# Performance work log

Measured on AMD Instinct MI355X. Metric: run time of the kernel, lower is better.

Reference implementation:

```python
import jax, jax.numpy as jnp
import numpy as np

GRID_SIZE = 4
ORDER = 3
NUM_BASIS = GRID_SIZE + ORDER  # 7
KNOTS = jnp.linspace(-1.0, 1.0, NUM_BASIS + ORDER + 1)  # 11 knots


def _normalise(x):
    # eval-mode with uninitialized running stats: use batch min/max
    min_val = x.min(axis=0)
    max_val = x.max(axis=0)
    width = jnp.maximum(max_val - min_val, 0.01)
    centre = 0.5 * (max_val + min_val)
    scaled = (x - centre) / (0.5 * width)
    return jnp.clip(scaled, -2.0, 2.0)


def _bspline_basis(x):
    # x: (B, I) -> basis: (B, I, NUM_BASIS), de Boor recursion vectorized over i
    xe = x[..., None]  # (B, I, 1)
    idx = jnp.arange(NUM_BASIS)
    left, right = KNOTS[idx], KNOTS[idx + 1]
    basis = ((xe >= left) & (xe < right)).astype(x.dtype)
    last = jnp.where(xe[..., 0] == KNOTS[NUM_BASIS], 1.0, basis[..., -1])
    basis = basis.at[..., -1].set(last)
    for k in range(1, ORDER + 1):
        d1 = KNOTS[idx + k] - KNOTS[idx]
        d2 = KNOTS[idx + k + 1] - KNOTS[idx + 1]
        b_next = jnp.concatenate([basis[..., 1:], jnp.zeros_like(basis[..., :1])], axis=-1)
        t1 = jnp.where(d1 > 0, (xe - KNOTS[idx]) / jnp.where(d1 > 0, d1, 1.0), 0.0) * basis
        t2 = jnp.where(d2 > 0, (KNOTS[idx + k + 1] - xe) / jnp.where(d2 > 0, d2, 1.0), 0.0) * b_next
        basis = t1 + t2
    return basis


def setup_inputs() -> dict:
    key = jax.random.key(0)
    k1, k2, k3 = jax.random.split(key, 3)
    B, I, O = 8192, 256, 256
    x = jax.random.normal(k1, (B, I), dtype=jnp.float32)
    # xavier-uniform base_weight
    bound = float(np.sqrt(6.0 / (I + O)))
    base_weight = jax.random.uniform(k2, (O, I), minval=-bound, maxval=bound, dtype=jnp.float32)
    spline_weight = jnp.ones((O, I), dtype=jnp.float32)
    spline_coeff = 0.001 * jax.random.normal(k3, (O, I, NUM_BASIS), dtype=jnp.float32)
    bias = jnp.zeros((O,), dtype=jnp.float32)
    return {"x": x, "base_weight": base_weight, "spline_weight": spline_weight,
            "spline_coeff": spline_coeff, "bias": bias}


def reference(x, base_weight, spline_weight, spline_coeff, bias):
    x_norm = _normalise(x)                          # (B, I)
    basis = _bspline_basis(x_norm)                  # (B, I, M)
    silu_x = x_norm * jax.nn.sigmoid(x_norm)        # (B, I)
    base_out = silu_x @ base_weight.T               # sum_i silu_i * W_oi -> (B, O)
    coeff_scaled = spline_coeff * spline_weight[..., None]  # (O, I, M)
    spline_out = jnp.einsum('bim,oim->bo', basis, coeff_scaled)
    return base_out + spline_out + bias[None, :]
```

## Files before the change

### kernel.cpp

```cpp
#include <hip/hip_runtime.h>
#include <hip/hip_bf16.h>

#define B_SZ 8192
#define I_SZ 256
#define O_SZ 256
#define KDIM 2048
#define BM 32
#define BN 128
#define BKT 64
#define NT 32

typedef __bf16 bf16x8 __attribute__((ext_vector_type(8)));
typedef float f32x4 __attribute__((ext_vector_type(4)));

__global__ __launch_bounds__(256) void minmax_partial(
    const float* __restrict__ x, float* __restrict__ pmin,
    float* __restrict__ pmax) {
  const int cg = threadIdx.x & 63;
  const int rs = threadIdx.x >> 6;
  const int r0 = blockIdx.x * 64;
  const float* p = x + (size_t)(r0 + rs) * I_SZ + cg * 4;
  float4 mn = {1e30f, 1e30f, 1e30f, 1e30f};
  float4 mx = {-1e30f, -1e30f, -1e30f, -1e30f};
#pragma unroll
  for (int k = 0; k < 16; ++k) {
    const float4 v = *reinterpret_cast<const float4*>(p + (size_t)k * 4 * I_SZ);
    mn.x = fminf(mn.x, v.x); mn.y = fminf(mn.y, v.y);
    mn.z = fminf(mn.z, v.z); mn.w = fminf(mn.w, v.w);
    mx.x = fmaxf(mx.x, v.x); mx.y = fmaxf(mx.y, v.y);
    mx.z = fmaxf(mx.z, v.z); mx.w = fmaxf(mx.w, v.w);
  }
  __shared__ float rmn[4][I_SZ], rmx[4][I_SZ];
  *reinterpret_cast<float4*>(&rmn[rs][cg * 4]) = mn;
  *reinterpret_cast<float4*>(&rmx[rs][cg * 4]) = mx;
  __syncthreads();
  if (threadIdx.x < 64) {
    float4 a, b;
    const int c0 = threadIdx.x * 4;
    a.x = fminf(fminf(rmn[0][c0+0], rmn[1][c0+0]), fminf(rmn[2][c0+0], rmn[3][c0+0]));
    a.y = fminf(fminf(rmn[0][c0+1], rmn[1][c0+1]), fminf(rmn[2][c0+1], rmn[3][c0+1]));
    a.z = fminf(fminf(rmn[0][c0+2], rmn[1][c0+2]), fminf(rmn[2][c0+2], rmn[3][c0+2]));
    a.w = fminf(fminf(rmn[0][c0+3], rmn[1][c0+3]), fminf(rmn[2][c0+3], rmn[3][c0+3]));
    b.x = fmaxf(fmaxf(rmx[0][c0+0], rmx[1][c0+0]), fmaxf(rmx[2][c0+0], rmx[3][c0+0]));
    b.y = fmaxf(fmaxf(rmx[0][c0+1], rmx[1][c0+1]), fmaxf(rmx[2][c0+1], rmx[3][c0+1]));
    b.z = fmaxf(fmaxf(rmx[0][c0+2], rmx[1][c0+2]), fmaxf(rmx[2][c0+2], rmx[3][c0+2]));
    b.w = fmaxf(fmaxf(rmx[0][c0+3], rmx[1][c0+3]), fmaxf(rmx[2][c0+3], rmx[3][c0+3]));
    *reinterpret_cast<float4*>(&pmin[blockIdx.x * I_SZ + c0]) = a;
    *reinterpret_cast<float4*>(&pmax[blockIdx.x * I_SZ + c0]) = b;
  }
}

__global__ void pack_W(const float* __restrict__ bw,
                       const float* __restrict__ sw,
                       const float* __restrict__ coeff,
                       __hip_bfloat16* __restrict__ W,
                       const float* __restrict__ pmin,
                       const float* __restrict__ pmax,
                       float* __restrict__ cenrhw) {
  const int idx = blockIdx.x * blockDim.x + threadIdx.x;
  const int i = idx & (I_SZ - 1);
  const int o = idx >> 8;
  const float s = sw[idx];
  union { __hip_bfloat16 h[8]; float4 f4; } u;
#pragma unroll
  for (int m = 0; m < 7; ++m)
    u.h[m] = __float2bfloat16(coeff[(size_t)idx * 7 + m] * s);
  u.h[7] = __float2bfloat16(bw[idx]);
  const size_t off = (size_t)o * KDIM + (size_t)((i ^ (o & 7)) << 3);
  *reinterpret_cast<float4*>(&W[off]) = u.f4;

  if (blockIdx.x == 0) {
    const int c = threadIdx.x;
    float mn = 1e30f, mx = -1e30f;
#pragma unroll 8
    for (int p = 0; p < 128; ++p) {
      mn = fminf(mn, pmin[p * I_SZ + c]);
      mx = fmaxf(mx, pmax[p * I_SZ + c]);
    }
    const float width = fmaxf(mx - mn, 0.01f);
    cenrhw[2 * c]     = 0.5f * (mx + mn);
    cenrhw[2 * c + 1] = 2.0f / width;
  }
}

__device__ __forceinline__ void async16(const __hip_bfloat16* g, __hip_bfloat16* l) {
  __builtin_amdgcn_global_load_lds(
      (const __attribute__((address_space(1))) void*)g,
      (__attribute__((address_space(3))) void*)l, 16, 0, 0);
}

__global__ __launch_bounds__(256, 2) void gemm_fused(
    const float* __restrict__ x, const __hip_bfloat16* __restrict__ W,
    const float* __restrict__ cenrhw, const float* __restrict__ bias,
    float* __restrict__ out) {
  __shared__ __align__(16) __hip_bfloat16 Alds[2][BM * BKT];
  __shared__ __align__(16) __hip_bfloat16 Blds[2][BN * BKT];
  __shared__ float2 scl[I_SZ];

  const int t = threadIdx.x;
  const int lane = t & 63;
  const int wave = t >> 6;
  const int fr = lane & 15, fk = lane >> 4;

  const int bid = blockIdx.x;
  const int swz = (bid & 7) * 64 + (bid >> 3);
  const int bm = swz >> 1, bn = swz & 1;
  const int r0 = bm * BM;
  const int c0 = bn * BN;

  scl[t] = reinterpret_cast<const float2*>(cenrhw)[t];

  const int arow = t >> 3;
  const int af_  = t & 7;
  const float* xp = x + (size_t)(r0 + arow) * I_SZ + af_;

  const __hip_bfloat16* gb0 = W + (size_t)(c0 + (t >> 3)) * KDIM + (t & 7) * 8;

  f32x4 acc[2][2] = {{{0.f,0.f,0.f,0.f},{0.f,0.f,0.f,0.f}},
                     {{0.f,0.f,0.f,0.f},{0.f,0.f,0.f,0.f}}};

  auto stageB = [&](int buf, int kt) {
    const size_t k0 = (size_t)kt * BKT;
    async16(gb0 + k0,                      &Blds[buf][t * 8]);
    async16(gb0 + k0 + (size_t)32 * KDIM,  &Blds[buf][2048 + t * 8]);
    async16(gb0 + k0 + (size_t)64 * KDIM,  &Blds[buf][4096 + t * 8]);
    async16(gb0 + k0 + (size_t)96 * KDIM,  &Blds[buf][6144 + t * 8]);
  };

  auto buildA = [&](int buf, int kt, float xv) {
    const int i = kt * 8 + af_;
    const float2 s = scl[i];
    float xn = (xv - s.x) * s.y;
    xn = fminf(fmaxf(xn, -2.0f), 2.0f);
    float d[11];
#pragma unroll
    for (int j = 0; j < 11; ++j) d[j] = xn - (-1.0f + 0.2f * j);
    float bas[7];
#pragma unroll
    for (int j = 0; j < 7; ++j)
      bas[j] = (d[j] >= 0.0f && d[j + 1] < 0.0f) ? 1.0f : 0.0f;
    if (d[7] == 0.0f) bas[6] = 1.0f;
#pragma unroll
    for (int k = 1; k <= 3; ++k) {
      const float rk = (k == 1) ? 5.0f : (k == 2) ? 2.5f : (1.0f / 0.6f);
#pragma unroll
      for (int j = 0; j < 7; ++j) {
        const float bn_ = (j < 6) ? bas[j + 1] : 0.0f;
        bas[j] = (d[j] * bas[j] - d[j + k + 1] * bn_) * rk;
      }
    }
    const float silu = xn / (1.0f + __expf(-xn));
    union { __hip_bfloat16 h[8]; float4 f4; } u;
#pragma unroll
    for (int m = 0; m < 7; ++m) u.h[m] = __float2bfloat16(bas[m]);
    u.h[7] = __float2bfloat16(silu);
    const int unit = af_ ^ (arow & 7);
    *reinterpret_cast<float4*>(&Alds[buf][arow * BKT + unit * 8]) = u.f4;
  };

  auto compute = [&](int buf) {
    bf16x8 af[2][2], bg[2][2];
#pragma unroll
    for (int m = 0; m < 2; ++m)
#pragma unroll
      for (int kk = 0; kk < 2; ++kk) {
        const int row = m * 16 + fr;
        const int unit = ((kk << 2) | fk) ^ (row & 7);
        af[m][kk] = *reinterpret_cast<const bf16x8*>(&Alds[buf][row * BKT + unit * 8]);
      }
#pragma unroll
    for (int n = 0; n < 2; ++n)
#pragma unroll
      for (int kk = 0; kk < 2; ++kk) {
        const int row = wave * 32 + n * 16 + fr;
        const int unit = ((kk << 2) | fk) ^ (row & 7);
        bg[n][kk] = *reinterpret_cast<const bf16x8*>(&Blds[buf][row * BKT + unit * 8]);
      }
#pragma unroll
    for (int kk = 0; kk < 2; ++kk)
#pragma unroll
      for (int m = 0; m < 2; ++m)
#pragma unroll
        for (int n = 0; n < 2; ++n)
          acc[m][n] = __builtin_amdgcn_mfma_f32_16x16x32_bf16(
              af[m][kk], bg[n][kk], acc[m][n], 0, 0, 0);
  };

  const float xv0 = xp[0];
  float xpf = xp[8];
  __syncthreads();
  stageB(0, 0);
  buildA(0, 0, xv0);
  __syncthreads();
  int cur = 0;
  for (int kt = 0; kt < NT - 1; ++kt) {
    stageB(cur ^ 1, kt + 1);
    float xpf2 = (kt + 2 < NT) ? xp[(kt + 2) * 8] : 0.0f;
    buildA(cur ^ 1, kt + 1, xpf);
    compute(cur);
    __syncthreads();
    xpf = xpf2;
    cur ^= 1;
  }
  compute(cur);

#pragma unroll
  for (int m = 0; m < 2; ++m)
#pragma unroll
    for (int n = 0; n < 2; ++n) {
      const int col = c0 + wave * 32 + n * 16 + fr;
      const float bc = bias[col];
#pragma unroll
      for (int r = 0; r < 4; ++r) {
        const int row = r0 + m * 16 + fk * 4 + r;
        out[(size_t)row * O_SZ + col] = acc[m][n][r] + bc;
      }
    }
}

extern "C" void kernel_launch(void* const* d_in, const int* in_sizes, int n_in,
                              void* d_out, int out_size, void* d_ws, size_t ws_size,
                              hipStream_t stream) {
  const float* x     = (const float*)d_in[0];
  const float* bw    = (const float*)d_in[1];
  const float* sw    = (const float*)d_in[2];
  const float* coeff = (const float*)d_in[3];
  const float* bias  = (const float*)d_in[4];
  float* out = (float*)d_out;

  char* ws = (char*)d_ws;
  __hip_bfloat16* Wbuf = (__hip_bfloat16*)ws;
  float* pmin   = (float*)(ws + (size_t)O_SZ * KDIM * 2);
  float* pmax   = pmin + 128 * I_SZ;
  float* cenrhw = pmax + 128 * I_SZ;

  minmax_partial<<<128, 256, 0, stream>>>(x, pmin, pmax);
  pack_W<<<(O_SZ * I_SZ) / 256, 256, 0, stream>>>(bw, sw, coeff, Wbuf,
                                                  pmin, pmax, cenrhw);
  gemm_fused<<<(B_SZ / BM) * (O_SZ / BN), 256, 0, stream>>>(x, Wbuf, cenrhw,
                                                            bias, out);
}
```

Measured before the change: 47.27 us.

## Use closed-form cubic B-spline, atomic min/max reduction, and lighter barriers

The de Boor recursion in the A-tile builder is replaced by a closed-form uniform cubic B-spline: the normalised value is mapped to a knot interval and the four nonzero basis weights are computed directly. The two-level min/max reduction becomes order-preserving integer atomics, which removes the serial final reduction from pack_W but adds two memsets. The K-loop's __syncthreads is replaced by explicit waitcnt plus s_barrier, which allows one outstanding global load to remain in flight. The aim is to cut ALU work in buildA and shorten the serial reduction step, at the risk of subtle edge-case differences at the clamp boundaries (for example x at exactly the last knot) and of synchronisation correctness.

```diff
diff --git a/kernel.cpp b/kernel.cpp
--- a/kernel.cpp
+++ b/kernel.cpp
@@ -13,9 +13,18 @@
 typedef __bf16 bf16x8 __attribute__((ext_vector_type(8)));
 typedef float f32x4 __attribute__((ext_vector_type(4)));
 
+__device__ __forceinline__ unsigned fkey(float f) {
+  unsigned u = __float_as_uint(f);
+  return (u & 0x80000000u) ? ~u : (u | 0x80000000u);
+}
+__device__ __forceinline__ float funkey(unsigned k) {
+  unsigned u = (k & 0x80000000u) ? (k ^ 0x80000000u) : ~k;
+  return __uint_as_float(u);
+}
+
 __global__ __launch_bounds__(256) void minmax_partial(
-    const float* __restrict__ x, float* __restrict__ pmin,
-    float* __restrict__ pmax) {
+    const float* __restrict__ x, unsigned* __restrict__ smin,
+    unsigned* __restrict__ smax) {
   const int cg = threadIdx.x & 63;
   const int rs = threadIdx.x >> 6;
   const int r0 = blockIdx.x * 64;
@@ -35,28 +44,23 @@
   *reinterpret_cast<float4*>(&rmx[rs][cg * 4]) = mx;
   __syncthreads();
   if (threadIdx.x < 64) {
-    float4 a, b;
-    const int c0 = threadIdx.x * 4;
-    a.x = fminf(fminf(rmn[0][c0+0], rmn[1][c0+0]), fminf(rmn[2][c0+0], rmn[3][c0+0]));
-    a.y = fminf(fminf(rmn[0][c0+1], rmn[1][c0+1]), fminf(rmn[2][c0+1], rmn[3][c0+1]));
-    a.z = fminf(fminf(rmn[0][c0+2], rmn[1][c0+2]), fminf(rmn[2][c0+2], rmn[3][c0+2]));
-    a.w = fminf(fminf(rmn[0][c0+3], rmn[1][c0+3]), fminf(rmn[2][c0+3], rmn[3][c0+3]));
-    b.x = fmaxf(fmaxf(rmx[0][c0+0], rmx[1][c0+0]), fmaxf(rmx[2][c0+0], rmx[3][c0+0]));
-    b.y = fmaxf(fmaxf(rmx[0][c0+1], rmx[1][c0+1]), fmaxf(rmx[2][c0+1], rmx[3][c0+1]));
-    b.z = fmaxf(fmaxf(rmx[0][c0+2], rmx[1][c0+2]), fmaxf(rmx[2][c0+2], rmx[3][c0+2]));
-    b.w = fmaxf(fmaxf(rmx[0][c0+3], rmx[1][c0+3]), fmaxf(rmx[2][c0+3], rmx[3][c0+3]));
-    *reinterpret_cast<float4*>(&pmin[blockIdx.x * I_SZ + c0]) = a;
-    *reinterpret_cast<float4*>(&pmax[blockIdx.x * I_SZ + c0]) = b;
+#pragma unroll
+    for (int c = 0; c < 4; ++c) {
+      const int col = threadIdx.x * 4 + c;
+      const float a = fminf(fminf(rmn[0][col], rmn[1][col]),
+                            fminf(rmn[2][col], rmn[3][col]));
+      const float b = fmaxf(fmaxf(rmx[0][col], rmx[1][col]),
+                            fmaxf(rmx[2][col], rmx[3][col]));
+      atomicMin(&smin[col], fkey(a));
+      atomicMax(&smax[col], fkey(b));
+    }
   }
 }
 
 __global__ void pack_W(const float* __restrict__ bw,
                        const float* __restrict__ sw,
                        const float* __restrict__ coeff,
-                       __hip_bfloat16* __restrict__ W,
-                       const float* __restrict__ pmin,
-                       const float* __restrict__ pmax,
-                       float* __restrict__ cenrhw) {
+                       __hip_bfloat16* __restrict__ W) {
   const int idx = blockIdx.x * blockDim.x + threadIdx.x;
   const int i = idx & (I_SZ - 1);
   const int o = idx >> 8;
@@ -68,19 +72,6 @@
   u.h[7] = __float2bfloat16(bw[idx]);
   const size_t off = (size_t)o * KDIM + (size_t)((i ^ (o & 7)) << 3);
   *reinterpret_cast<float4*>(&W[off]) = u.f4;
-
-  if (blockIdx.x == 0) {
-    const int c = threadIdx.x;
-    float mn = 1e30f, mx = -1e30f;
-#pragma unroll 8
-    for (int p = 0; p < 128; ++p) {
-      mn = fminf(mn, pmin[p * I_SZ + c]);
-      mx = fmaxf(mx, pmax[p * I_SZ + c]);
-    }
-    const float width = fmaxf(mx - mn, 0.01f);
-    cenrhw[2 * c]     = 0.5f * (mx + mn);
-    cenrhw[2 * c + 1] = 2.0f / width;
-  }
 }
 
 __device__ __forceinline__ void async16(const __hip_bfloat16* g, __hip_bfloat16* l) {
@@ -91,8 +82,8 @@
 
 __global__ __launch_bounds__(256, 2) void gemm_fused(
     const float* __restrict__ x, const __hip_bfloat16* __restrict__ W,
-    const float* __restrict__ cenrhw, const float* __restrict__ bias,
-    float* __restrict__ out) {
+    const unsigned* __restrict__ smin, const unsigned* __restrict__ smax,
+    const float* __restrict__ bias, float* __restrict__ out) {
   __shared__ __align__(16) __hip_bfloat16 Alds[2][BM * BKT];
   __shared__ __align__(16) __hip_bfloat16 Blds[2][BN * BKT];
   __shared__ float2 scl[I_SZ];
@@ -108,7 +99,13 @@
   const int r0 = bm * BM;
   const int c0 = bn * BN;
 
-  scl[t] = reinterpret_cast<const float2*>(cenrhw)[t];
+  {
+    const float mn = funkey(smin[t]);
+    const float mx = funkey(smax[t]);
+    const float w = fmaxf(mx - mn, 0.01f);
+    const float rhw = 2.0f / w;
+    scl[t] = make_float2(rhw, -0.5f * (mx + mn) * rhw);
+  }
 
   const int arow = t >> 3;
   const int af_  = t & 7;
@@ -128,37 +125,43 @@
   };
 
   auto buildA = [&](int buf, int kt, float xv) {
-    const int i = kt * 8 + af_;
-    const float2 s = scl[i];
-    float xn = (xv - s.x) * s.y;
-    xn = fminf(fmaxf(xn, -2.0f), 2.0f);
-    float d[11];
-#pragma unroll
-    for (int j = 0; j < 11; ++j) d[j] = xn - (-1.0f + 0.2f * j);
-    float bas[7];
-#pragma unroll
-    for (int j = 0; j < 7; ++j)
-      bas[j] = (d[j] >= 0.0f && d[j + 1] < 0.0f) ? 1.0f : 0.0f;
-    if (d[7] == 0.0f) bas[6] = 1.0f;
-#pragma unroll
-    for (int k = 1; k <= 3; ++k) {
-      const float rk = (k == 1) ? 5.0f : (k == 2) ? 2.5f : (1.0f / 0.6f);
-#pragma unroll
-      for (int j = 0; j < 7; ++j) {
-        const float bn_ = (j < 6) ? bas[j + 1] : 0.0f;
-        bas[j] = (d[j] * bas[j] - d[j + k + 1] * bn_) * rk;
-      }
+    const float2 s2 = scl[kt * 8 + af_];
+    const float xn = __builtin_fmaf(xv, s2.x, s2.y);
+    const float sp = __builtin_fmaf(xn, 5.0f, 5.0f);
+    const float cf = floorf(sp);
+    const float c6 = fminf(cf, 6.0f);
+    const int ci = (int)c6;
+    const float u = sp - c6;
+    const float zm = (sp > 7.0f) ? 0.0f : (1.0f / 6.0f);
+    const float u2 = u * u;
+    const float u3 = u2 * u;
+    const float t1 = 1.0f - u;
+    const float q3 = u3 * zm;
+    const float q0 = (t1 * t1) * (t1 * zm);
+    float h2 = __builtin_fmaf(-3.0f, u, 3.0f);
+    h2 = __builtin_fmaf(h2, u, 3.0f);
+    h2 = __builtin_fmaf(h2, u, 1.0f);
+    const float q2 = h2 * zm;
+    float h1 = __builtin_fmaf(3.0f, u, -6.0f);
+    h1 = __builtin_fmaf(h1, u2, 4.0f);
+    const float q1 = h1 * zm;
+    const float silu = xn * __builtin_amdgcn_rcpf(1.0f + __expf(-xn));
+    union { __hip_bfloat16 h[8]; float4 f4; } uu;
+#pragma unroll
+    for (int j = 0; j < 7; ++j) {
+      float v = 0.0f;
+      v = (ci == j + 3) ? q0 : v;
+      v = (ci == j + 2) ? q1 : v;
+      v = (ci == j + 1) ? q2 : v;
+      v = (ci == j)     ? q3 : v;
+      uu.h[j] = __float2bfloat16(v);
     }
-    const float silu = xn / (1.0f + __expf(-xn));
-    union { __hip_bfloat16 h[8]; float4 f4; } u;
-#pragma unroll
-    for (int m = 0; m < 7; ++m) u.h[m] = __float2bfloat16(bas[m]);
-    u.h[7] = __float2bfloat16(silu);
+    uu.h[7] = __float2bfloat16(silu);
     const int unit = af_ ^ (arow & 7);
-    *reinterpret_cast<float4*>(&Alds[buf][arow * BKT + unit * 8]) = u.f4;
+    *reinterpret_cast<float4*>(&Alds[buf][arow * BKT + unit * 8]) = uu.f4;
   };
 
-  auto compute = [&](int buf) {
+  auto compute = [&](int bbuf, int abuf) {
     bf16x8 af[2][2], bg[2][2];
 #pragma unroll
     for (int m = 0; m < 2; ++m)
@@ -166,7 +169,7 @@
       for (int kk = 0; kk < 2; ++kk) {
         const int row = m * 16 + fr;
         const int unit = ((kk << 2) | fk) ^ (row & 7);
-        af[m][kk] = *reinterpret_cast<const bf16x8*>(&Alds[buf][row * BKT + unit * 8]);
+        af[m][kk] = *reinterpret_cast<const bf16x8*>(&Alds[abuf][row * BKT + unit * 8]);
       }
 #pragma unroll
     for (int n = 0; n < 2; ++n)
@@ -174,7 +177,7 @@
       for (int kk = 0; kk < 2; ++kk) {
         const int row = wave * 32 + n * 16 + fr;
         const int unit = ((kk << 2) | fk) ^ (row & 7);
-        bg[n][kk] = *reinterpret_cast<const bf16x8*>(&Blds[buf][row * BKT + unit * 8]);
+        bg[n][kk] = *reinterpret_cast<const bf16x8*>(&Blds[bbuf][row * BKT + unit * 8]);
       }
 #pragma unroll
     for (int kk = 0; kk < 2; ++kk)
@@ -187,22 +190,26 @@
   };
 
   const float xv0 = xp[0];
-  float xpf = xp[8];
   __syncthreads();
   stageB(0, 0);
+  float xpf = xp[8];
   buildA(0, 0, xv0);
-  __syncthreads();
-  int cur = 0;
+  asm volatile("s_waitcnt vmcnt(1) lgkmcnt(0)" ::: "memory");
+  __builtin_amdgcn_s_barrier();
+  asm volatile("" ::: "memory");
+
   for (int kt = 0; kt < NT - 1; ++kt) {
-    stageB(cur ^ 1, kt + 1);
-    float xpf2 = (kt + 2 < NT) ? xp[(kt + 2) * 8] : 0.0f;
-    buildA(cur ^ 1, kt + 1, xpf);
-    compute(cur);
-    __syncthreads();
+    const int cb = kt & 1, nb = cb ^ 1;
+    stageB(nb, kt + 1);
+    const float xpf2 = xp[min(kt + 2, NT - 1) * 8];
+    buildA(nb, kt + 1, xpf);
     xpf = xpf2;
-    cur ^= 1;
-  }
-  compute(cur);
+    compute(cb, cb);
+    asm volatile("s_waitcnt vmcnt(1) lgkmcnt(0)" ::: "memory");
+    __builtin_amdgcn_s_barrier();
+    asm volatile("" ::: "memory");
+  }
+  compute((NT - 1) & 1, (NT - 1) & 1);
 
 #pragma unroll
   for (int m = 0; m < 2; ++m)
@@ -230,13 +237,14 @@
 
   char* ws = (char*)d_ws;
   __hip_bfloat16* Wbuf = (__hip_bfloat16*)ws;
-  float* pmin   = (float*)(ws + (size_t)O_SZ * KDIM * 2);
-  float* pmax   = pmin + 128 * I_SZ;
-  float* cenrhw = pmax + 128 * I_SZ;
-
-  minmax_partial<<<128, 256, 0, stream>>>(x, pmin, pmax);
-  pack_W<<<(O_SZ * I_SZ) / 256, 256, 0, stream>>>(bw, sw, coeff, Wbuf,
-                                                  pmin, pmax, cenrhw);
-  gemm_fused<<<(B_SZ / BM) * (O_SZ / BN), 256, 0, stream>>>(x, Wbuf, cenrhw,
-                                                            bias, out);
-}
+  unsigned* smin = (unsigned*)(ws + (size_t)O_SZ * KDIM * 2);
+  unsigned* smax = smin + I_SZ;
+
+  hipMemsetAsync(smin, 0xFF, I_SZ * sizeof(unsigned), stream);
+  hipMemsetAsync(smax, 0x00, I_SZ * sizeof(unsigned), stream);
+
+  minmax_partial<<<128, 256, 0, stream>>>(x, smin, smax);
+  pack_W<<<(O_SZ * I_SZ) / 256, 256, 0, stream>>>(bw, sw, coeff, Wbuf);
+  gemm_fused<<<(B_SZ / BM) * (O_SZ / BN), 256, 0, stream>>>(x, Wbuf, smin,
+                                                            smax, bias, out);
+}
```

Result: slower. 51.61 us (+9.2%).
